# Kernel optimization log

Hardware: AMD Instinct MI355X
Metric: run time of the kernel (lower is better)

Reference implementation:

```python
import jax, jax.numpy as jnp
import numpy as np

NEG = -1e9  # large negative for masked attention logits (stands in for -inf in init_inf)


def setup_inputs() -> dict:
    B, T, D, H = 64, 128, 512, 512
    key = jax.random.key(0)
    ks = jax.random.split(key, 20)
    s = lambda fan: 1.0 / np.sqrt(fan)
    inp = {
        "inputs": jax.random.normal(ks[0], (B, T, D), jnp.float32),
        "h0": jax.random.normal(ks[1], (B, H), jnp.float32),
        "c0": jax.random.normal(ks[2], (B, H), jnp.float32),
        "candidate": jax.random.normal(ks[3], (B, T, H), jnp.float32),
        "candidate_mask": jnp.ones((B, T), jnp.float32),
        # learned parameters
        "input0": jax.random.uniform(ks[4], (D,), jnp.float32, -1.0, 1.0),
        "W_ih": jax.random.uniform(ks[5], (4 * H, D), jnp.float32, -s(D), s(D)),
        "b_ih": jax.random.uniform(ks[6], (4 * H,), jnp.float32, -s(D), s(D)),
        "W_hh": jax.random.uniform(ks[7], (4 * H, H), jnp.float32, -s(H), s(H)),
        "b_hh": jax.random.uniform(ks[8], (4 * H,), jnp.float32, -s(H), s(H)),
        "W_out": jax.random.uniform(ks[9], (H, 2 * H), jnp.float32, -s(2 * H), s(2 * H)),
        "b_out": jax.random.uniform(ks[10], (H,), jnp.float32, -s(2 * H), s(2 * H)),
        "W_inp": jax.random.uniform(ks[11], (H, H), jnp.float32, -s(H), s(H)),
        "b_inp": jax.random.uniform(ks[12], (H,), jnp.float32, -s(H), s(H)),
        "W_ctx": jax.random.uniform(ks[13], (H, H), jnp.float32, -s(H), s(H)),
        "b_ctx": jax.random.uniform(ks[14], (H,), jnp.float32, -s(H), s(H)),
        "v": jax.random.uniform(ks[15], (H,), jnp.float32, -s(H), s(H)),
    }
    return inp


def _decode(inputs, h0, c0, candidate, candidate_mask, input0,
            W_ih, b_ih, W_hh, b_hh, W_out, b_out, W_inp, b_inp, W_ctx, b_ctx, v):
    B, T, D = inputs.shape
    mask0 = candidate_mask.astype(jnp.float32)
    max_len = mask0.sum(axis=-1)  # [B]
    # context projection is step-invariant: precompute once
    ctx_lin = jnp.einsum("bth,gh->btg", candidate, W_ctx) + b_ctx  # [B,T,H]
    pos = jnp.arange(T)

    def step(carry, cur_len):
        h, c, mask, x = carry
        # LSTM cell
        gates = x @ W_ih.T + b_ih + h @ W_hh.T + b_hh  # [B,4H]
        gi, gf, gg, go = jnp.split(gates, 4, axis=1)
        c_t = jax.nn.sigmoid(gf) * c + jax.nn.sigmoid(gi) * jnp.tanh(gg)
        h_lstm = jax.nn.sigmoid(go) * jnp.tanh(c_t)
        # FFN (Bahdanau) attention: e = v . tanh(W_inp h + W_ctx ctx)
        inp = h_lstm @ W_inp.T + b_inp  # [B,H]
        e = jnp.einsum("h,bth->bt", v, jnp.tanh(ctx_lin + inp[:, None, :]))  # [B,T]
        scores = jnp.where(mask > 0, e, NEG)  # masked logits (init_inf masking)
        alpha = jax.nn.softmax(scores, axis=-1)
        attn = jnp.einsum("bt,bth->bh", alpha, ctx_lin)
        h_t = jnp.tanh(jnp.concatenate([attn, h_lstm], axis=1) @ W_out.T + b_out)
        # pointer selection
        probs = alpha * mask  # softmax(scores) * mask
        sel = jnp.argmax(probs, axis=1)
        sel = jnp.where(max_len > cur_len, sel, cur_len)
        one_hot = (pos[None, :] == sel[:, None]).astype(jnp.float32)
        mask = mask * (1.0 - one_hot)  # repeat=False: remove chosen position
        x_next = jnp.einsum("bt,btd->bd", one_hot, inputs)  # gather selected input
        return (h_t, c_t, mask, x_next), (scores, sel)

    x0 = jnp.broadcast_to(input0, (B, D))
    (h_f, c_f, _, _), (scores_all, ptrs) = jax.lax.scan(
        step, (h0, c0, mask0, x0), jnp.arange(T))
    outputs = jnp.transpose(scores_all, (1, 0, 2))  # [B,T,T]
    pointers = ptrs.T  # [B,T]
    return outputs, pointers, h_f, c_f


def reference(inputs, h0, c0, candidate, candidate_mask, input0,
              W_ih, b_ih, W_hh, b_hh, W_out, b_out, W_inp, b_inp, W_ctx, b_ctx, v):
    return _decode(inputs, h0, c0, candidate, candidate_mask, input0,
                   W_ih, b_ih, W_hh, b_hh, W_out, b_out, W_inp, b_inp, W_ctx, b_ctx, v)
```

## Files before the change

kernel.cpp:

```cpp
#include <hip/hip_runtime.h>
#include <cstddef>
#include <cstdint>


#define NEGV (-1e9f)

static constexpr int T = 128;
static constexpr int NB = 256, NTHR = 256;
static constexpr int NG = 4, GBLK = 64, BG = 16;

static constexpr size_t OFF_SYNC = 0;
static constexpr size_t OFF_H    = 512;
static constexpr size_t OFF_C    = OFF_H    + 64*512;
static constexpr size_t OFF_HL   = OFF_C    + 64*512;
static constexpr size_t OFF_INP  = OFF_HL   + 64*512;
static constexpr size_t OFF_HW   = OFF_INP  + 64*512;
static constexpr size_t OFF_E    = OFF_HW   + 64*512;
static constexpr size_t OFF_MASK = OFF_E    + 64*128;
static constexpr size_t OFF_ML   = OFF_MASK + 64*128;
static constexpr size_t OFF_SEL  = OFF_ML   + 64;
static constexpr size_t OFF_X0W  = OFF_SEL  + 64;
static constexpr size_t OFF_XW   = OFF_X0W  + 2048;
static constexpr size_t OFF_CTX  = OFF_XW   + (size_t)8192*2048;
static constexpr size_t OFF_CWO  = OFF_CTX  + (size_t)8192*512;

__device__ __forceinline__ float sigf(float x) { return 1.0f / (1.0f + expf(-x)); }

__device__ __forceinline__ void gridbar(int* gflags, int* gepoch, int target, int gl, int t) {
  __syncthreads();
  if (t == 0) {
    __hip_atomic_store(&gflags[gl], target, __ATOMIC_RELEASE, __HIP_MEMORY_SCOPE_AGENT);
  }
  if (gl == 0) {
    if (t < 64) {
      int miss = 0;
      for (;;) {
        int f = __hip_atomic_load(&gflags[t], __ATOMIC_RELAXED, __HIP_MEMORY_SCOPE_AGENT);
        if (__all(f >= target)) break;
        __builtin_amdgcn_s_sleep(1);
        if (++miss > 50000000) break;
      }
      if (t == 0)
        __hip_atomic_store(gepoch, target, __ATOMIC_RELEASE, __HIP_MEMORY_SCOPE_AGENT);
    }
  } else {
    if (t == 0) {
      int miss = 0;
      while (__hip_atomic_load(gepoch, __ATOMIC_RELAXED, __HIP_MEMORY_SCOPE_AGENT) < target) {
        __builtin_amdgcn_s_sleep(2);
        if (++miss > 50000000) break;
      }
    }
  }
  __syncthreads();
  __builtin_amdgcn_fence(__ATOMIC_ACQUIRE, "agent");
}

__global__ __launch_bounds__(256) void x0w_kernel(
    const float* __restrict__ input0, const float* __restrict__ W_ih,
    const float* __restrict__ b_ih, const float* __restrict__ b_hh,
    float* __restrict__ x0w) {
  int wid = (blockIdx.x * 256 + threadIdx.x) >> 6;
  int l = threadIdx.x & 63;
  const float* wr = W_ih + (size_t)wid * 512;
  float acc = 0.f;
  #pragma unroll
  for (int q = 0; q < 8; ++q) acc += input0[l*8+q] * wr[l*8+q];
  #pragma unroll
  for (int off = 32; off; off >>= 1) acc += __shfl_xor(acc, off, 64);
  if (l == 0) x0w[wid] = acc + b_ih[wid] + b_hh[wid];
}

__global__ __launch_bounds__(256) void gemm_abt(
    const float* __restrict__ A, const float* __restrict__ Bm,
    const float* __restrict__ bias1, const float* __restrict__ bias2,
    float* __restrict__ C, int M, int N, int K, int ldb) {
  __shared__ float As[16][132];
  __shared__ float Bs[16][132];
  const int t = threadIdx.x;
  const int tx = t & 15, ty = t >> 4;
  const int mbase = blockIdx.y * 128, nbase = blockIdx.x * 128;
  float acc[8][8] = {};
  for (int kc = 0; kc < K; kc += 16) {
    __syncthreads();
    #pragma unroll
    for (int r = 0; r < 2; ++r) {
      int q = r * 256 + t;
      int row = q >> 2, kq = (q & 3) * 4;
      float4 va = *(const float4*)&A[(size_t)(mbase + row) * K + kc + kq];
      As[kq+0][row] = va.x; As[kq+1][row] = va.y; As[kq+2][row] = va.z; As[kq+3][row] = va.w;
      float4 vb = *(const float4*)&Bm[(size_t)(nbase + row) * ldb + kc + kq];
      Bs[kq+0][row] = vb.x; Bs[kq+1][row] = vb.y; Bs[kq+2][row] = vb.z; Bs[kq+3][row] = vb.w;
    }
    __syncthreads();
    #pragma unroll
    for (int kk = 0; kk < 16; ++kk) {
      float a[8], b[8];
      *(float4*)(a)   = *(const float4*)&As[kk][ty*8];
      *(float4*)(a+4) = *(const float4*)&As[kk][ty*8+4];
      *(float4*)(b)   = *(const float4*)&Bs[kk][tx*8];
      *(float4*)(b+4) = *(const float4*)&Bs[kk][tx*8+4];
      #pragma unroll
      for (int i = 0; i < 8; ++i)
        #pragma unroll
        for (int j = 0; j < 8; ++j)
          acc[i][j] = fmaf(a[i], b[j], acc[i][j]);
    }
  }
  float bv[8];
  #pragma unroll
  for (int q = 0; q < 8; ++q) {
    int n = nbase + tx*8 + q;
    bv[q] = (bias1 ? bias1[n] : 0.f) + (bias2 ? bias2[n] : 0.f);
  }
  #pragma unroll
  for (int i = 0; i < 8; ++i) {
    size_t m = (size_t)(mbase + ty*8 + i);
    float4 o0 = make_float4(acc[i][0]+bv[0], acc[i][1]+bv[1], acc[i][2]+bv[2], acc[i][3]+bv[3]);
    float4 o1 = make_float4(acc[i][4]+bv[4], acc[i][5]+bv[5], acc[i][6]+bv[6], acc[i][7]+bv[7]);
    *(float4*)&C[m * N + nbase + tx*8]     = o0;
    *(float4*)&C[m * N + nbase + tx*8 + 4] = o1;
  }
}

__global__ __launch_bounds__(256) void decoder_kernel(
    const float* __restrict__ h0, const float* __restrict__ c0,
    const float* __restrict__ cmask,
    const float* __restrict__ W_hh,
    const float* __restrict__ W_inp, const float* __restrict__ b_inp_,
    const float* __restrict__ W_out, const float* __restrict__ b_out_,
    const float* __restrict__ vvec,
    float* __restrict__ ws, float* __restrict__ out) {
  __shared__ float swA[32*576];
  __shared__ float swB[16*576];
  __shared__ float sph[512];
  __shared__ float sbias[16];

  int* syncp = (int*)ws;
  float* hrow  = ws + OFF_H;
  float* crow  = ws + OFF_C;
  float* hlrow = ws + OFF_HL;
  float* inpp  = ws + OFF_INP;
  float* hwp   = ws + OFF_HW;
  float* ep    = ws + OFF_E;
  float* maskp = ws + OFF_MASK;
  float* mlp   = ws + OFF_ML;
  int*   selp  = (int*)(ws + OFF_SEL);
  const float* x0wp = ws + OFF_X0W;
  const float* xwp  = ws + OFF_XW;
  const float* ctxp = ws + OFF_CTX;
  const float* cwop = ws + OFF_CWO;

  float* out_scores = out;
  float* out_ptrs   = out + (size_t)64*128*128;
  float* out_hf     = out_ptrs + 64*128;
  float* out_cf     = out_hf + 64*512;

  const int g = blockIdx.x, t = threadIdx.x;
  const int gg = g >> 6, gl = g & 63;
  const int w = t >> 6, l = t & 63;
  const int bl = t >> 4, js = t & 15;
  int* gflags = syncp + gg * 64;
  int* gepoch = syncp + 256 + gg * 32;
  int bar = 0;

  {
    const int a = t >> 3, seg = t & 7;
    const int gate = a >> 3, rl = a & 7;
    const float* srcrow = W_hh + ((size_t)(gate*512 + gl*8 + rl)) * 512;
    #pragma unroll
    for (int c2 = 0; c2 < 2; ++c2) {
      const int ch = seg*2 + c2;
      const float4* s4 = (const float4*)&srcrow[ch*32];
      float4* d4 = (float4*)&swA[a*576 + ch*36];
      #pragma unroll
      for (int u = 0; u < 8; ++u) d4[u] = s4[u];
    }
    const int a2 = t >> 4, seg2 = t & 15;
    const float* srcrow2 = (a2 < 8) ? (W_inp + (size_t)(gl*8 + a2) * 512)
                                    : (W_out + (size_t)(gl*8 + a2 - 8) * 1024 + 512);
    const float4* s42 = (const float4*)&srcrow2[seg2*32];
    float4* d42 = (float4*)&swB[a2*576 + seg2*36];
    #pragma unroll
    for (int u = 0; u < 8; ++u) d42[u] = s42[u];
    if (t < 16) sbias[t] = (t < 8) ? b_inp_[gl*8 + t] : b_out_[gl*8 + t - 8];
  }

  {
    const int idx = gl * NTHR + t;
    const int base = gg * 8192;
    if (idx < 8192) hrow[base + idx] = h0[base + idx];
    else            crow[base + idx - 8192] = c0[base + idx - 8192];
    if (idx < 2048) maskp[gg*2048 + idx] = cmask[gg*2048 + idx];
    if (gl == 0 && t < BG) {
      float s_ = 0.f;
      for (int q = 0; q < 128; ++q) s_ += cmask[(gg*BG + t)*128 + q];
      mlp[gg*BG + t] = s_;
    }
  }
  gridbar(gflags, gepoch, ++bar, gl, t);

  float vreg[8];
  *(float4*)(vreg)   = *(const float4*)&vvec[l*8];
  *(float4*)(vreg+4) = *(const float4*)&vvec[l*8+4];

  for (int s = 0; s < T; ++s) {
    {
      const int b = gg*BG + bl;
      const float* hb = hrow + (size_t)b*512 + js*32;
      float hbuf[32];
      #pragma unroll
      for (int q = 0; q < 8; ++q) *(float4*)&hbuf[q*4] = *(const float4*)&hb[q*4];
      float acc[32];
      #pragma unroll
      for (int a = 0; a < 32; ++a) acc[a] = 0.f;
      const float* wbase = &swA[js*36];
      #pragma unroll
      for (int a = 0; a < 32; ++a) {
        const float* wr = wbase + a*576;
        #pragma unroll
        for (int j = 0; j < 32; j += 4) {
          float4 wv = *(const float4*)&wr[j];
          acc[a] = fmaf(hbuf[j+0], wv.x, fmaf(hbuf[j+1], wv.y,
                   fmaf(hbuf[j+2], wv.z, fmaf(hbuf[j+3], wv.w, acc[a]))));
        }
      }
      #pragma unroll
      for (int a = 0; a < 32; ++a) {
        acc[a] += __shfl_xor(acc[a], 1, 64);
        acc[a] += __shfl_xor(acc[a], 2, 64);
        acc[a] += __shfl_xor(acc[a], 4, 64);
        acc[a] += __shfl_xor(acc[a], 8, 64);
      }
      if (js == 0) {
        #pragma unroll
        for (int a = 0; a < 32; ++a) sph[bl*32 + a] = acc[a];
      }
      __syncthreads();
      if (js < 8) {
        const int r = gl*8 + js;
        float pi = sph[bl*32 + 0*8 + js];
        float pf = sph[bl*32 + 1*8 + js];
        float pg = sph[bl*32 + 2*8 + js];
        float po = sph[bl*32 + 3*8 + js];
        const float* xrow = (s == 0) ? x0wp
                          : (xwp + ((size_t)b*128 + (size_t)selp[b]) * 2048);
        float gi  = pi + xrow[0*512 + r];
        float gf  = pf + xrow[1*512 + r];
        float gg2 = pg + xrow[2*512 + r];
        float go  = po + xrow[3*512 + r];
        float cp = crow[(size_t)b*512 + r];
        float ct = sigf(gf)*cp + sigf(gi)*tanhf(gg2);
        crow[(size_t)b*512 + r] = ct;
        hlrow[(size_t)b*512 + r] = sigf(go)*tanhf(ct);
      }
    }
    gridbar(gflags, gepoch, ++bar, gl, t);

    {
      const int b = gg*BG + bl;
      const float* hb = hlrow + (size_t)b*512 + js*32;
      float hbuf[32];
      #pragma unroll
      for (int q = 0; q < 8; ++q) *(float4*)&hbuf[q*4] = *(const float4*)&hb[q*4];
      float acc[16];
      #pragma unroll
      for (int a = 0; a < 16; ++a) acc[a] = 0.f;
      const float* wbase = &swB[js*36];
      #pragma unroll
      for (int a = 0; a < 16; ++a) {
        const float* wr = wbase + a*576;
        #pragma unroll
        for (int j = 0; j < 32; j += 4) {
          float4 wv = *(const float4*)&wr[j];
          acc[a] = fmaf(hbuf[j+0], wv.x, fmaf(hbuf[j+1], wv.y,
                   fmaf(hbuf[j+2], wv.z, fmaf(hbuf[j+3], wv.w, acc[a]))));
        }
      }
      #pragma unroll
      for (int a = 0; a < 16; ++a) {
        acc[a] += __shfl_xor(acc[a], 1, 64);
        acc[a] += __shfl_xor(acc[a], 2, 64);
        acc[a] += __shfl_xor(acc[a], 4, 64);
        acc[a] += __shfl_xor(acc[a], 8, 64);
      }
      if (js == 0) {
        #pragma unroll
        for (int a = 0; a < 16; ++a) sph[bl*16 + a] = acc[a];
      }
      __syncthreads();
      if (js < 8) {
        const int r = gl*8 + js;
        inpp[(size_t)b*512 + r] = sph[bl*16 + js]     + sbias[js];
        hwp [(size_t)b*512 + r] = sph[bl*16 + 8 + js] + sbias[8 + js];
      }
    }
    gridbar(gflags, gepoch, ++bar, gl, t);

    {
      const int b_ = gg*BG + (gl >> 2);
      const int tbase = (gl & 3)*32 + w*8;
      float ii[8];
      *(float4*)(ii)   = *(const float4*)&inpp[(size_t)b_*512 + l*8];
      *(float4*)(ii+4) = *(const float4*)&inpp[(size_t)b_*512 + l*8 + 4];
      #pragma unroll
      for (int q = 0; q < 8; ++q) {
        int tc = tbase + q;
        const float* cr = ctxp + ((size_t)(b_*128 + tc))*512 + l*8;
        float4 c0_ = *(const float4*)cr;
        float4 c1_ = *(const float4*)(cr + 4);
        float acc = vreg[0]*tanhf(c0_.x + ii[0]) + vreg[1]*tanhf(c0_.y + ii[1])
                  + vreg[2]*tanhf(c0_.z + ii[2]) + vreg[3]*tanhf(c0_.w + ii[3])
                  + vreg[4]*tanhf(c1_.x + ii[4]) + vreg[5]*tanhf(c1_.y + ii[5])
                  + vreg[6]*tanhf(c1_.z + ii[6]) + vreg[7]*tanhf(c1_.w + ii[7]);
        #pragma unroll
        for (int off = 32; off; off >>= 1) acc += __shfl_xor(acc, off, 64);
        if (l == 0) {
          float mk = maskp[b_*128 + tc];
          float sc = (mk > 0.f) ? acc : NEGV;
          ep[b_*128 + tc] = sc;
          out_scores[((size_t)b_*128 + s)*128 + tc] = sc;
        }
      }
    }
    gridbar(gflags, gepoch, ++bar, gl, t);

    {
      const int b_ = gg*BG + (gl >> 2), is = (gl & 3) << 7;
      if (w == 0) {
        float s0 = ep[b_*128 + l], s1 = ep[b_*128 + 64 + l];
        float mx = fmaxf(s0, s1);
        #pragma unroll
        for (int off = 32; off; off >>= 1) mx = fmaxf(mx, __shfl_xor(mx, off, 64));
        float x0 = expf(s0 - mx), x1 = expf(s1 - mx);
        float sum = x0 + x1;
        #pragma unroll
        for (int off = 32; off; off >>= 1) sum += __shfl_xor(sum, off, 64);
        float a0 = x0 / sum, a1 = x1 / sum;
        sph[l] = a0; sph[64 + l] = a1;
        if ((gl & 3) == 0) {
          float m0 = maskp[b_*128 + l], m1 = maskp[b_*128 + 64 + l];
          float p0 = a0 * m0, p1 = a1 * m1;
          float pv; int pi;
          if (p1 > p0) { pv = p1; pi = l + 64; } else { pv = p0; pi = l; }
          #pragma unroll
          for (int off = 32; off; off >>= 1) {
            float ov = __shfl_xor(pv, off, 64);
            int   oi = __shfl_xor(pi, off, 64);
            if (ov > pv || (ov == pv && oi < pi)) { pv = ov; pi = oi; }
          }
          if (l == 0) {
            int se = (mlp[b_] > (float)s) ? pi : s;
            selp[b_] = se;
            maskp[b_*128 + se] = 0.f;
            out_ptrs[b_*128 + s] = (float)se;
          }
        }
      }
      __syncthreads();
      {
        const int io = t & 127, half = t >> 7;
        const int i = is + io;
        const float* aw = &sph[half * 64];
        const float* cw = cwop + ((size_t)(b_*128 + half*64))*512 + i;
        float acc0 = 0.f, acc1 = 0.f, acc2 = 0.f, acc3 = 0.f;
        #pragma unroll 8
        for (int tc = 0; tc < 64; tc += 4) {
          acc0 = fmaf(aw[tc+0], cw[(size_t)(tc+0)*512], acc0);
          acc1 = fmaf(aw[tc+1], cw[(size_t)(tc+1)*512], acc1);
          acc2 = fmaf(aw[tc+2], cw[(size_t)(tc+2)*512], acc2);
          acc3 = fmaf(aw[tc+3], cw[(size_t)(tc+3)*512], acc3);
        }
        sph[128 + t] = (acc0 + acc1) + (acc2 + acc3);
      }
      __syncthreads();
      if (t < 128) {
        const int i = is + t;
        float tot = hwp[(size_t)b_*512 + i] + sph[128 + t] + sph[256 + t];
        hrow[(size_t)b_*512 + i] = tanhf(tot);
      }
    }
    gridbar(gflags, gepoch, ++bar, gl, t);
  }

  {
    const int idx = gl * NTHR + t;
    const int base = gg * 8192;
    if (idx < 8192) out_hf[base + idx] = hrow[base + idx];
    else            out_cf[base + idx - 8192] = crow[base + idx - 8192];
  }
}

extern "C" void kernel_launch(void* const* d_in, const int* in_sizes, int n_in,
                              void* d_out, int out_size, void* d_ws, size_t ws_size,
                              hipStream_t stream) {
  (void)in_sizes; (void)n_in; (void)out_size; (void)ws_size;
  const float* inputs    = (const float*)d_in[0];
  const float* h0        = (const float*)d_in[1];
  const float* c0        = (const float*)d_in[2];
  const float* candidate = (const float*)d_in[3];
  const float* cmask     = (const float*)d_in[4];
  const float* input0    = (const float*)d_in[5];
  const float* W_ih      = (const float*)d_in[6];
  const float* b_ih      = (const float*)d_in[7];
  const float* W_hh      = (const float*)d_in[8];
  const float* b_hh      = (const float*)d_in[9];
  const float* W_out     = (const float*)d_in[10];
  const float* b_out     = (const float*)d_in[11];
  const float* W_inp     = (const float*)d_in[12];
  const float* b_inp     = (const float*)d_in[13];
  const float* W_ctx     = (const float*)d_in[14];
  const float* b_ctx     = (const float*)d_in[15];
  const float* v         = (const float*)d_in[16];
  float* ws  = (float*)d_ws;
  float* outp = (float*)d_out;

  (void)hipMemsetAsync(d_ws, 0, 2048, stream);

  x0w_kernel<<<512, 256, 0, stream>>>(input0, W_ih, b_ih, b_hh, ws + OFF_X0W);

  gemm_abt<<<dim3(16, 64), 256, 0, stream>>>(inputs, W_ih, b_ih, b_hh,
                                             ws + OFF_XW, 8192, 2048, 512, 512);
  gemm_abt<<<dim3(4, 64), 256, 0, stream>>>(candidate, W_ctx, b_ctx, nullptr,
                                            ws + OFF_CTX, 8192, 512, 512, 512);
  gemm_abt<<<dim3(4, 64), 256, 0, stream>>>(ws + OFF_CTX, W_out, nullptr, nullptr,
                                            ws + OFF_CWO, 8192, 512, 512, 1024);

  decoder_kernel<<<NB, NTHR, 0, stream>>>(h0, c0, cmask, W_hh, W_inp, b_inp,
                                          W_out, b_out, v, ws, outp);
}
```

Baseline: 9.697 ms.

## Merge attention score and pointer phases per batch row, drop one grid barrier

Each batch row's attention scores, softmax, argmax and context combine now run inside a single block (16 blocks per group), keeping the mask and scores in shared memory. This removes one of the four grid barriers per step and the global score and mask buffers. The barrier becomes a flat all-to-all flag poll with system-scope relaxed atomics for shared state, replacing the fence, and the inner dot products use two accumulators. The cost is that only 16 of 64 blocks do the attention phase, each with 4x the work, and the atomic 8-byte loads may be slower than plain vector loads.

```diff
diff --git a/kernel.cpp b/kernel.cpp
--- a/kernel.cpp
+++ b/kernel.cpp
@@ -7,53 +7,55 @@
 
 static constexpr int T = 128;
 static constexpr int NB = 256, NTHR = 256;
-static constexpr int NG = 4, GBLK = 64, BG = 16;
-
-static constexpr size_t OFF_SYNC = 0;
+static constexpr int BG = 16;
+
+static constexpr size_t OFF_FLAGS = 0;
+static constexpr size_t OFF_SEL  = 256;
 static constexpr size_t OFF_H    = 512;
 static constexpr size_t OFF_C    = OFF_H    + 64*512;
 static constexpr size_t OFF_HL   = OFF_C    + 64*512;
 static constexpr size_t OFF_INP  = OFF_HL   + 64*512;
 static constexpr size_t OFF_HW   = OFF_INP  + 64*512;
-static constexpr size_t OFF_E    = OFF_HW   + 64*512;
-static constexpr size_t OFF_MASK = OFF_E    + 64*128;
-static constexpr size_t OFF_ML   = OFF_MASK + 64*128;
-static constexpr size_t OFF_SEL  = OFF_ML   + 64;
-static constexpr size_t OFF_X0W  = OFF_SEL  + 64;
+static constexpr size_t OFF_X0W  = OFF_HW   + 64*512;
 static constexpr size_t OFF_XW   = OFF_X0W  + 2048;
 static constexpr size_t OFF_CTX  = OFF_XW   + (size_t)8192*2048;
 static constexpr size_t OFF_CWO  = OFF_CTX  + (size_t)8192*512;
 
 __device__ __forceinline__ float sigf(float x) { return 1.0f / (1.0f + expf(-x)); }
 
-__device__ __forceinline__ void gridbar(int* gflags, int* gepoch, int target, int gl, int t) {
+__device__ __forceinline__ float aload(const float* p) {
+  return __hip_atomic_load(p, __ATOMIC_RELAXED, __HIP_MEMORY_SCOPE_SYSTEM);
+}
+__device__ __forceinline__ void astore(float* p, float v) {
+  __hip_atomic_store(p, v, __ATOMIC_RELAXED, __HIP_MEMORY_SCOPE_SYSTEM);
+}
+__device__ __forceinline__ float2 aload2(const float* p) {
+  union { unsigned long long u; float2 f; } c;
+  c.u = __hip_atomic_load((const unsigned long long*)p, __ATOMIC_RELAXED,
+                          __HIP_MEMORY_SCOPE_SYSTEM);
+  return c.f;
+}
+__device__ __forceinline__ void astore2(float* p, float2 v) {
+  union { unsigned long long u; float2 f; } c; c.f = v;
+  __hip_atomic_store((unsigned long long*)p, c.u, __ATOMIC_RELAXED,
+                     __HIP_MEMORY_SCOPE_SYSTEM);
+}
+
+__device__ __forceinline__ void gridbar(int* gflags, int target, int gl, int t) {
   __syncthreads();
-  if (t == 0) {
-    __hip_atomic_store(&gflags[gl], target, __ATOMIC_RELEASE, __HIP_MEMORY_SCOPE_AGENT);
-  }
-  if (gl == 0) {
-    if (t < 64) {
-      int miss = 0;
-      for (;;) {
-        int f = __hip_atomic_load(&gflags[t], __ATOMIC_RELAXED, __HIP_MEMORY_SCOPE_AGENT);
-        if (__all(f >= target)) break;
-        __builtin_amdgcn_s_sleep(1);
-        if (++miss > 50000000) break;
-      }
-      if (t == 0)
-        __hip_atomic_store(gepoch, target, __ATOMIC_RELEASE, __HIP_MEMORY_SCOPE_AGENT);
-    }
-  } else {
-    if (t == 0) {
-      int miss = 0;
-      while (__hip_atomic_load(gepoch, __ATOMIC_RELAXED, __HIP_MEMORY_SCOPE_AGENT) < target) {
-        __builtin_amdgcn_s_sleep(2);
-        if (++miss > 50000000) break;
-      }
+  if (t == 0)
+    __hip_atomic_store(&gflags[gl], target, __ATOMIC_RELEASE, __HIP_MEMORY_SCOPE_SYSTEM);
+  if (t < 64) {
+    int miss = 0;
+    for (;;) {
+      int f = __hip_atomic_load(&gflags[t], __ATOMIC_RELAXED, __HIP_MEMORY_SCOPE_SYSTEM);
+      if (__all(f >= target)) break;
+      __builtin_amdgcn_s_sleep(1);
+      if (++miss > 100000000) break;
     }
   }
   __syncthreads();
-  __builtin_amdgcn_fence(__ATOMIC_ACQUIRE, "agent");
+  asm volatile("" ::: "memory");
 }
 
 __global__ __launch_bounds__(256) void x0w_kernel(
@@ -134,18 +136,17 @@
   __shared__ float swA[32*576];
   __shared__ float swB[16*576];
   __shared__ float sph[512];
+  __shared__ float smask[128];
   __shared__ float sbias[16];
-
-  int* syncp = (int*)ws;
+  __shared__ float s_mlen;
+
+  int* flagsp = (int*)ws;
+  int* selp   = (int*)(ws + OFF_SEL);
   float* hrow  = ws + OFF_H;
   float* crow  = ws + OFF_C;
   float* hlrow = ws + OFF_HL;
   float* inpp  = ws + OFF_INP;
   float* hwp   = ws + OFF_HW;
-  float* ep    = ws + OFF_E;
-  float* maskp = ws + OFF_MASK;
-  float* mlp   = ws + OFF_ML;
-  int*   selp  = (int*)(ws + OFF_SEL);
   const float* x0wp = ws + OFF_X0W;
   const float* xwp  = ws + OFF_XW;
   const float* ctxp = ws + OFF_CTX;
@@ -160,9 +161,9 @@
   const int gg = g >> 6, gl = g & 63;
   const int w = t >> 6, l = t & 63;
   const int bl = t >> 4, js = t & 15;
-  int* gflags = syncp + gg * 64;
-  int* gepoch = syncp + 256 + gg * 32;
+  int* gflags = flagsp + gg * 64;
   int bar = 0;
+  const int bCD = gg*BG + gl;
 
   {
     const int a = t >> 3, seg = t & 7;
@@ -189,16 +190,26 @@
   {
     const int idx = gl * NTHR + t;
     const int base = gg * 8192;
-    if (idx < 8192) hrow[base + idx] = h0[base + idx];
-    else            crow[base + idx - 8192] = c0[base + idx - 8192];
-    if (idx < 2048) maskp[gg*2048 + idx] = cmask[gg*2048 + idx];
-    if (gl == 0 && t < BG) {
-      float s_ = 0.f;
-      for (int q = 0; q < 128; ++q) s_ += cmask[(gg*BG + t)*128 + q];
-      mlp[gg*BG + t] = s_;
-    }
-  }
-  gridbar(gflags, gepoch, ++bar, gl, t);
+    if (idx < 4096) {
+      const float2 v = *(const float2*)&h0[base + idx*2];
+      astore2(&hrow[base + idx*2], v);
+    }
+    if (t < 128) {
+      const int bb = gg*BG + (t >> 3), rr = gl*8 + (t & 7);
+      crow[(size_t)bb*512 + rr] = c0[(size_t)bb*512 + rr];
+    }
+    if (gl < BG) {
+      if (t < 128) smask[t] = cmask[bCD*128 + t];
+      __syncthreads();
+      if (t < 64) {
+        float m_ = smask[t] + smask[64 + t];
+        #pragma unroll
+        for (int off = 32; off; off >>= 1) m_ += __shfl_xor(m_, off, 64);
+        if (t == 0) s_mlen = m_;
+      }
+    }
+  }
+  gridbar(gflags, ++bar, gl, t);
 
   float vreg[8];
   *(float4*)(vreg)   = *(const float4*)&vvec[l*8];
@@ -210,20 +221,23 @@
       const float* hb = hrow + (size_t)b*512 + js*32;
       float hbuf[32];
       #pragma unroll
-      for (int q = 0; q < 8; ++q) *(float4*)&hbuf[q*4] = *(const float4*)&hb[q*4];
+      for (int q = 0; q < 16; ++q) *(float2*)&hbuf[q*2] = aload2(&hb[q*2]);
       float acc[32];
-      #pragma unroll
-      for (int a = 0; a < 32; ++a) acc[a] = 0.f;
       const float* wbase = &swA[js*36];
       #pragma unroll
       for (int a = 0; a < 32; ++a) {
         const float* wr = wbase + a*576;
-        #pragma unroll
-        for (int j = 0; j < 32; j += 4) {
-          float4 wv = *(const float4*)&wr[j];
-          acc[a] = fmaf(hbuf[j+0], wv.x, fmaf(hbuf[j+1], wv.y,
-                   fmaf(hbuf[j+2], wv.z, fmaf(hbuf[j+3], wv.w, acc[a]))));
-        }
+        float s0 = 0.f, s1 = 0.f;
+        #pragma unroll
+        for (int j = 0; j < 32; j += 8) {
+          float4 w0 = *(const float4*)&wr[j];
+          float4 w1 = *(const float4*)&wr[j+4];
+          s0 = fmaf(hbuf[j+0], w0.x, fmaf(hbuf[j+1], w0.y,
+               fmaf(hbuf[j+2], w0.z, fmaf(hbuf[j+3], w0.w, s0))));
+          s1 = fmaf(hbuf[j+4], w1.x, fmaf(hbuf[j+5], w1.y,
+               fmaf(hbuf[j+6], w1.z, fmaf(hbuf[j+7], w1.w, s1))));
+        }
+        acc[a] = s0 + s1;
       }
       #pragma unroll
       for (int a = 0; a < 32; ++a) {
@@ -243,8 +257,12 @@
         float pf = sph[bl*32 + 1*8 + js];
         float pg = sph[bl*32 + 2*8 + js];
         float po = sph[bl*32 + 3*8 + js];
-        const float* xrow = (s == 0) ? x0wp
-                          : (xwp + ((size_t)b*128 + (size_t)selp[b]) * 2048);
+        const float* xrow;
+        if (s == 0) xrow = x0wp;
+        else {
+          int se = __hip_atomic_load(&selp[b], __ATOMIC_RELAXED, __HIP_MEMORY_SCOPE_SYSTEM);
+          xrow = xwp + ((size_t)b*128 + (size_t)se) * 2048;
+        }
         float gi  = pi + xrow[0*512 + r];
         float gf  = pf + xrow[1*512 + r];
         float gg2 = pg + xrow[2*512 + r];
@@ -252,30 +270,33 @@
         float cp = crow[(size_t)b*512 + r];
         float ct = sigf(gf)*cp + sigf(gi)*tanhf(gg2);
         crow[(size_t)b*512 + r] = ct;
-        hlrow[(size_t)b*512 + r] = sigf(go)*tanhf(ct);
-      }
-    }
-    gridbar(gflags, gepoch, ++bar, gl, t);
+        astore(&hlrow[(size_t)b*512 + r], sigf(go)*tanhf(ct));
+      }
+    }
+    gridbar(gflags, ++bar, gl, t);
 
     {
       const int b = gg*BG + bl;
       const float* hb = hlrow + (size_t)b*512 + js*32;
       float hbuf[32];
       #pragma unroll
-      for (int q = 0; q < 8; ++q) *(float4*)&hbuf[q*4] = *(const float4*)&hb[q*4];
+      for (int q = 0; q < 16; ++q) *(float2*)&hbuf[q*2] = aload2(&hb[q*2]);
       float acc[16];
-      #pragma unroll
-      for (int a = 0; a < 16; ++a) acc[a] = 0.f;
       const float* wbase = &swB[js*36];
       #pragma unroll
       for (int a = 0; a < 16; ++a) {
         const float* wr = wbase + a*576;
-        #pragma unroll
-        for (int j = 0; j < 32; j += 4) {
-          float4 wv = *(const float4*)&wr[j];
-          acc[a] = fmaf(hbuf[j+0], wv.x, fmaf(hbuf[j+1], wv.y,
-                   fmaf(hbuf[j+2], wv.z, fmaf(hbuf[j+3], wv.w, acc[a]))));
-        }
+        float s0 = 0.f, s1 = 0.f;
+        #pragma unroll
+        for (int j = 0; j < 32; j += 8) {
+          float4 w0 = *(const float4*)&wr[j];
+          float4 w1 = *(const float4*)&wr[j+4];
+          s0 = fmaf(hbuf[j+0], w0.x, fmaf(hbuf[j+1], w0.y,
+               fmaf(hbuf[j+2], w0.z, fmaf(hbuf[j+3], w0.w, s0))));
+          s1 = fmaf(hbuf[j+4], w1.x, fmaf(hbuf[j+5], w1.y,
+               fmaf(hbuf[j+6], w1.z, fmaf(hbuf[j+7], w1.w, s1))));
+        }
+        acc[a] = s0 + s1;
       }
       #pragma unroll
       for (int a = 0; a < 16; ++a) {
@@ -291,22 +312,22 @@
       __syncthreads();
       if (js < 8) {
         const int r = gl*8 + js;
-        inpp[(size_t)b*512 + r] = sph[bl*16 + js]     + sbias[js];
-        hwp [(size_t)b*512 + r] = sph[bl*16 + 8 + js] + sbias[8 + js];
-      }
-    }
-    gridbar(gflags, gepoch, ++bar, gl, t);
-
-    {
-      const int b_ = gg*BG + (gl >> 2);
-      const int tbase = (gl & 3)*32 + w*8;
+        astore(&inpp[(size_t)b*512 + r], sph[bl*16 + js]     + sbias[js]);
+        astore(&hwp [(size_t)b*512 + r], sph[bl*16 + 8 + js] + sbias[8 + js]);
+      }
+    }
+    gridbar(gflags, ++bar, gl, t);
+
+    if (gl < BG) {
+      const int b = bCD;
       float ii[8];
-      *(float4*)(ii)   = *(const float4*)&inpp[(size_t)b_*512 + l*8];
-      *(float4*)(ii+4) = *(const float4*)&inpp[(size_t)b_*512 + l*8 + 4];
-      #pragma unroll
-      for (int q = 0; q < 8; ++q) {
-        int tc = tbase + q;
-        const float* cr = ctxp + ((size_t)(b_*128 + tc))*512 + l*8;
+      *(float2*)(ii)   = aload2(&inpp[(size_t)b*512 + l*8]);
+      *(float2*)(ii+2) = aload2(&inpp[(size_t)b*512 + l*8 + 2]);
+      *(float2*)(ii+4) = aload2(&inpp[(size_t)b*512 + l*8 + 4]);
+      *(float2*)(ii+6) = aload2(&inpp[(size_t)b*512 + l*8 + 6]);
+      for (int q = 0; q < 32; ++q) {
+        const int tc = w*32 + q;
+        const float* cr = ctxp + ((size_t)(b*128 + tc))*512 + l*8;
         float4 c0_ = *(const float4*)cr;
         float4 c1_ = *(const float4*)(cr + 4);
         float acc = vreg[0]*tanhf(c0_.x + ii[0]) + vreg[1]*tanhf(c0_.y + ii[1])
@@ -315,20 +336,12 @@
                   + vreg[6]*tanhf(c1_.z + ii[6]) + vreg[7]*tanhf(c1_.w + ii[7]);
         #pragma unroll
         for (int off = 32; off; off >>= 1) acc += __shfl_xor(acc, off, 64);
-        if (l == 0) {
-          float mk = maskp[b_*128 + tc];
-          float sc = (mk > 0.f) ? acc : NEGV;
-          ep[b_*128 + tc] = sc;
-          out_scores[((size_t)b_*128 + s)*128 + tc] = sc;
-        }
-      }
-    }
-    gridbar(gflags, gepoch, ++bar, gl, t);
-
-    {
-      const int b_ = gg*BG + (gl >> 2), is = (gl & 3) << 7;
+        if (l == 0) sph[tc] = (smask[tc] > 0.f) ? acc : NEGV;
+      }
+      __syncthreads();
+      if (t < 128) out_scores[((size_t)b*128 + s)*128 + t] = sph[t];
       if (w == 0) {
-        float s0 = ep[b_*128 + l], s1 = ep[b_*128 + 64 + l];
+        float s0 = sph[l], s1 = sph[64 + l];
         float mx = fmaxf(s0, s1);
         #pragma unroll
         for (int off = 32; off; off >>= 1) mx = fmaxf(mx, __shfl_xor(mx, off, 64));
@@ -337,57 +350,63 @@
         #pragma unroll
         for (int off = 32; off; off >>= 1) sum += __shfl_xor(sum, off, 64);
         float a0 = x0 / sum, a1 = x1 / sum;
-        sph[l] = a0; sph[64 + l] = a1;
-        if ((gl & 3) == 0) {
-          float m0 = maskp[b_*128 + l], m1 = maskp[b_*128 + 64 + l];
-          float p0 = a0 * m0, p1 = a1 * m1;
-          float pv; int pi;
-          if (p1 > p0) { pv = p1; pi = l + 64; } else { pv = p0; pi = l; }
-          #pragma unroll
-          for (int off = 32; off; off >>= 1) {
-            float ov = __shfl_xor(pv, off, 64);
-            int   oi = __shfl_xor(pi, off, 64);
-            if (ov > pv || (ov == pv && oi < pi)) { pv = ov; pi = oi; }
-          }
-          if (l == 0) {
-            int se = (mlp[b_] > (float)s) ? pi : s;
-            selp[b_] = se;
-            maskp[b_*128 + se] = 0.f;
-            out_ptrs[b_*128 + s] = (float)se;
-          }
+        sph[128 + l] = a0; sph[192 + l] = a1;
+        float p0 = a0 * smask[l], p1 = a1 * smask[64 + l];
+        float pv; int pi;
+        if (p1 > p0) { pv = p1; pi = l + 64; } else { pv = p0; pi = l; }
+        #pragma unroll
+        for (int off = 32; off; off >>= 1) {
+          float ov = __shfl_xor(pv, off, 64);
+          int   oi = __shfl_xor(pi, off, 64);
+          if (ov > pv || (ov == pv && oi < pi)) { pv = ov; pi = oi; }
+        }
+        if (l == 0) {
+          int se = (s_mlen > (float)s) ? pi : s;
+          __hip_atomic_store(&selp[b], se, __ATOMIC_RELAXED, __HIP_MEMORY_SCOPE_SYSTEM);
+          smask[se] = 0.f;
+          out_ptrs[b*128 + s] = (float)se;
         }
       }
       __syncthreads();
       {
-        const int io = t & 127, half = t >> 7;
-        const int i = is + io;
-        const float* aw = &sph[half * 64];
-        const float* cw = cwop + ((size_t)(b_*128 + half*64))*512 + i;
-        float acc0 = 0.f, acc1 = 0.f, acc2 = 0.f, acc3 = 0.f;
+        const int i0 = t*2;
+        const float* cw = cwop + (size_t)b*128*512 + i0;
+        float ax0=0.f, ax1=0.f, ax2=0.f, ax3=0.f;
+        float ay0=0.f, ay1=0.f, ay2=0.f, ay3=0.f;
         #pragma unroll 8
-        for (int tc = 0; tc < 64; tc += 4) {
-          acc0 = fmaf(aw[tc+0], cw[(size_t)(tc+0)*512], acc0);
-          acc1 = fmaf(aw[tc+1], cw[(size_t)(tc+1)*512], acc1);
-          acc2 = fmaf(aw[tc+2], cw[(size_t)(tc+2)*512], acc2);
-          acc3 = fmaf(aw[tc+3], cw[(size_t)(tc+3)*512], acc3);
-        }
-        sph[128 + t] = (acc0 + acc1) + (acc2 + acc3);
-      }
-      __syncthreads();
-      if (t < 128) {
-        const int i = is + t;
-        float tot = hwp[(size_t)b_*512 + i] + sph[128 + t] + sph[256 + t];
-        hrow[(size_t)b_*512 + i] = tanhf(tot);
-      }
-    }
-    gridbar(gflags, gepoch, ++bar, gl, t);
+        for (int tc = 0; tc < 128; tc += 4) {
+          float2 c0v = *(const float2*)&cw[(size_t)(tc+0)*512];
+          float2 c1v = *(const float2*)&cw[(size_t)(tc+1)*512];
+          float2 c2v = *(const float2*)&cw[(size_t)(tc+2)*512];
+          float2 c3v = *(const float2*)&cw[(size_t)(tc+3)*512];
+          float al0 = sph[128+tc+0], al1 = sph[128+tc+1];
+          float al2 = sph[128+tc+2], al3 = sph[128+tc+3];
+          ax0 = fmaf(al0, c0v.x, ax0); ay0 = fmaf(al0, c0v.y, ay0);
+          ax1 = fmaf(al1, c1v.x, ax1); ay1 = fmaf(al1, c1v.y, ay1);
+          ax2 = fmaf(al2, c2v.x, ax2); ay2 = fmaf(al2, c2v.y, ay2);
+          ax3 = fmaf(al3, c3v.x, ax3); ay3 = fmaf(al3, c3v.y, ay3);
+        }
+        float2 hwv = aload2(&hwp[(size_t)b*512 + i0]);
+        float2 hv;
+        hv.x = tanhf(hwv.x + ((ax0 + ax1) + (ax2 + ax3)));
+        hv.y = tanhf(hwv.y + ((ay0 + ay1) + (ay2 + ay3)));
+        astore2(&hrow[(size_t)b*512 + i0], hv);
+      }
+    }
+    gridbar(gflags, ++bar, gl, t);
   }
 
   {
     const int idx = gl * NTHR + t;
     const int base = gg * 8192;
-    if (idx < 8192) out_hf[base + idx] = hrow[base + idx];
-    else            out_cf[base + idx - 8192] = crow[base + idx - 8192];
+    if (idx < 4096) {
+      float2 v = aload2(&hrow[base + idx*2]);
+      *(float2*)&out_hf[base + idx*2] = v;
+    }
+    if (t < 128) {
+      const int bb = gg*BG + (t >> 3), rr = gl*8 + (t & 7);
+      out_cf[(size_t)bb*512 + rr] = crow[(size_t)bb*512 + rr];
+    }
   }
 }
 
```

Result: no change. 9.803 ms (+1.1%).
